# Optimization experiments

Hardware: AMD Instinct MI355X
Metric: run time of the kernel (lower is better)

The kernel has to match this reference:

```python
import jax, jax.numpy as jnp
import numpy as np

SIGMA = 16
P = 2 * SIGMA + 1  # 33x33 patch
OUT = 128          # feature_extractor.output_size
DN = ('NCHW', 'OIHW', 'NCHW')


def setup_inputs() -> dict:
    key = jax.random.key(0)
    ks = jax.random.split(key, 10)
    B, K, H, W = 4, 64, 256, 256
    images_ground = jax.random.normal(ks[0], (B, 3, H, W), jnp.float32)
    images_satellite = jax.random.normal(ks[1], (B, 3, H, W), jnp.float32)
    # normalized keypoints kept in interior so sigma-window crops stay in-bounds
    keypoints_ground = 0.2 + 0.6 * jax.random.uniform(ks[2], (B, K, 2), jnp.float32)
    keypoints_satellite = 0.2 + 0.6 * jax.random.uniform(ks[3], (B, K, 2), jnp.float32)
    # small CNN feature extractor params (conv 3->32 s1, conv 32->64 s2, GAP, linear 64->OUT)
    w1 = jax.random.normal(ks[4], (32, 3, 3, 3), jnp.float32) * 0.1
    b1 = jnp.zeros((32,), jnp.float32)
    w2 = jax.random.normal(ks[5], (64, 32, 3, 3), jnp.float32) * 0.05
    b2 = jnp.zeros((64,), jnp.float32)
    wl = jax.random.normal(ks[6], (OUT, 64), jnp.float32) * 0.1
    bl = jnp.zeros((OUT,), jnp.float32)
    return dict(images_ground=images_ground, images_satellite=images_satellite,
                keypoints_ground=keypoints_ground, keypoints_satellite=keypoints_satellite,
                w1=w1, b1=b1, w2=w2, b2=b2, wl=wl, bl=bl, num_samples=K)


def _cnn(x, w1, b1, w2, b2, wl, bl):
    # x: [M, 3, P, P] -> [M, OUT]
    h = jax.lax.conv_general_dilated(x, w1, (1, 1), 'VALID', dimension_numbers=DN)
    h = jax.nn.relu(h + b1[None, :, None, None])
    h = jax.lax.conv_general_dilated(h, w2, (2, 2), 'VALID', dimension_numbers=DN)
    h = jax.nn.relu(h + b2[None, :, None, None])
    h = h.mean(axis=(2, 3))  # global average pool -> [M, 64]
    return h @ wl.T + bl


def _crop_all(images, kps_px):
    # images: [B,3,H,W]; kps_px: [N,2] pixel (x, y) coords -> patches [N,B,3,P,P]
    B = images.shape[0]
    hw = images.shape[-1]
    starts = jnp.clip(jnp.floor(kps_px).astype(jnp.int32) - SIGMA, 0, hw - P)
    def one(st):
        return jax.lax.dynamic_slice(images, (0, 0, st[1], st[0]), (B, 3, P, P))
    return jax.vmap(one)(starts)


def reference(images_ground, images_satellite, keypoints_ground, keypoints_satellite,
              w1, b1, w2, b2, wl, bl, num_samples):
    kg = (keypoints_ground * images_ground.shape[-1]).reshape(-1, 2)   # [N,2]
    ksat = (keypoints_satellite * images_satellite.shape[-1]).reshape(-1, 2)
    pg = _crop_all(images_ground, kg)        # [N,B,3,P,P]
    ps = _crop_all(images_satellite, ksat)   # [N,B,3,P,P]
    N, B = pg.shape[0], pg.shape[1]
    fg = _cnn(pg.reshape(N * B, 3, P, P), w1, b1, w2, b2, wl, bl)
    fs = _cnn(ps.reshape(N * B, 3, P, P), w1, b1, w2, b2, wl, bl)
    fg = fg.reshape(N, B, OUT).transpose(1, 0, 2)  # features_ground [B,N,OUT]
    fs = fs.reshape(N, B, OUT).transpose(1, 0, 2)
    return jnp.mean((fg - fs) ** 2)
```

## Files before the change

kernel.cpp:

```cpp
#include <hip/hip_runtime.h>

#define HW   256
#define Pp   33
#define PPAD 36
#define OUTF 128
#define SIG  16

#define KCP   40
#define PLROW (2 * 16 * KCP)
#define PLSZ  (6 * PLROW)
#define IMS   40

#define WS_W1FH 0
#define WS_W1FL 512
#define WS_BHI  1024
#define WS_BLO  10240
#define WS_WLT  19456

typedef __attribute__((ext_vector_type(8))) short v8s;
typedef __attribute__((ext_vector_type(4))) short v4s;
typedef __attribute__((ext_vector_type(4))) float f32x4;

__device__ __forceinline__ unsigned short f2bf_rne(float x) {
  unsigned u = __float_as_uint(x);
  unsigned r = (u + 0x7FFFu + ((u >> 16) & 1u)) >> 16;
  return (unsigned short)r;
}
__device__ __forceinline__ float bf2f(unsigned short h) {
  return __uint_as_float(((unsigned)h) << 16);
}

__global__ __launch_bounds__(256) void prep_kernel(
    const float* __restrict__ w1, const float* __restrict__ w2,
    const float* __restrict__ wl, float* __restrict__ ws,
    float* __restrict__ out) {
  int t = blockIdx.x * 256 + threadIdx.x;
  int stride = gridDim.x * 256;
  if (blockIdx.x == 0 && threadIdx.x == 0) out[0] = 0.0f;
  unsigned short* w1h = (unsigned short*)(ws + WS_W1FH);
  unsigned short* w1lo = (unsigned short*)(ws + WS_W1FL);
  for (int i = t; i < 1024; i += stride) {
    int j  = i & 7;
    int l  = (i >> 3) & 63;
    int nt = i >> 9;
    int k  = 8 * (l >> 4) + j;
    int ch = 16 * nt + (l & 15);
    float v = (k < 27) ? w1[ch * 27 + k] : 0.0f;
    unsigned short h = f2bf_rne(v);
    w1h[i]  = h;
    w1lo[i] = f2bf_rne(v - bf2f(h));
  }
  unsigned short* bhi = (unsigned short*)(ws + WS_BHI);
  unsigned short* blo = (unsigned short*)(ws + WS_BLO);
  for (int i = t; i < 18432; i += stride) {
    int j  = i & 7;
    int l  = (i >> 3) & 63;
    int w  = (i >> 9) & 3;
    int tp = i >> 11;
    int ch = w * 16 + (l & 15);
    int kc = ((l >> 4) << 3) + j;
    int ky = tp / 3, kx = tp - ky * 3;
    float v = w2[ch * 288 + kc * 9 + ky * 3 + kx];
    unsigned short h = f2bf_rne(v);
    bhi[i] = h;
    blo[i] = f2bf_rne(v - bf2f(h));
  }
  for (int i = t; i < 8192; i += stride) {
    int o = i & 127, ii = i >> 7;
    ws[WS_WLT + i] = wl[o * 64 + ii];
  }
}

__global__ __launch_bounds__(256) void patch_cnn_kernel(
    const float* __restrict__ imgG, const float* __restrict__ imgS,
    const float* __restrict__ kpG,  const float* __restrict__ kpS,
    const float* __restrict__ b1g,  const float* __restrict__ b2g,
    const float* __restrict__ blg,  const float* __restrict__ ws,
    float* __restrict__ out) {
  __shared__ __align__(16) unsigned short patch[3 * Pp * PPAD];
  __shared__ __align__(16) unsigned short imcol[4][32 * IMS];
  __shared__ __align__(16) unsigned short hiP[PLSZ];
  __shared__ float gapv[64];
  __shared__ float fstash[OUTF];
  __shared__ float lred[4];

  const int bid  = blockIdx.x;
  const int n    = bid >> 2;
  const int b    = bid & 3;
  const int tid  = threadIdx.x;
  const int wave = tid >> 6;
  const int lane = tid & 63;

  const int m16 = lane & 15;
  const int qq  = lane >> 4;
  const int mt  = wave & 1;
  const int nt  = wave >> 1;

  const int bm = tid & 31;
  const int kq = tid >> 5;
  int  boff[4];
  bool bval[4];
#pragma unroll
  for (int j = 0; j < 4; ++j) {
    int k = 4 * kq + j;
    bval[j] = (k < 27);
    int kk = bval[j] ? k : 0;
    int ci = kk / 9, r2 = kk - ci * 9, ky = r2 / 3, kx = r2 - ky * 3;
    boff[j] = (ci * Pp + ky) * PPAD + bm + kx;
  }

  const v8s w1hF = ((const v8s*)((const unsigned short*)(ws + WS_W1FH)))[nt * 64 + lane];
  const v8s w1lF = ((const v8s*)((const unsigned short*)(ws + WS_W1FL)))[nt * 64 + lane];
  const float4 b1q = *(const float4*)&b1g[16 * nt + 4 * qq];

  const v8s* bhW = (const v8s*)((const unsigned short*)(ws + WS_BHI)) + (wave * 64 + lane);
  const v8s* blW = (const v8s*)((const unsigned short*)(ws + WS_BLO)) + (wave * 64 + lane);
  const float b2v = b2g[wave * 16 + m16];

  auto build_row = [&](int r, int d) {
    unsigned short h[4];
#pragma unroll
    for (int j = 0; j < 4; ++j)
      h[j] = bval[j] ? patch[boff[j] + r * PPAD] : (unsigned short)0;
    unsigned w0 = (unsigned)h[0] | ((unsigned)h[1] << 16);
    unsigned w1_ = (unsigned)h[2] | ((unsigned)h[3] << 16);
    *(uint2*)&imcol[d][bm * IMS + 4 * kq] = make_uint2(w0, w1_);
  };

  auto conv1_pair = [&](int bp, int r0) {
#pragma unroll
    for (int rr = 0; rr < 2; ++rr) {
      const int row = r0 + rr;
      if (row <= 30) {
        int sl = row % 6;
        v8s af = *(const v8s*)&imcol[2 * bp + rr][(16 * mt + m16) * IMS + 8 * qq];
        f32x4 a1 = {0.f, 0.f, 0.f, 0.f};
        a1 = __builtin_amdgcn_mfma_f32_16x16x32_bf16(w1hF, af, a1, 0, 0, 0);
        a1 = __builtin_amdgcn_mfma_f32_16x16x32_bf16(w1lF, af, a1, 0, 0, 0);
        const int x = 16 * mt + m16;
        v4s hv;
        hv[0] = (short)f2bf_rne(fmaxf(a1.x + b1q.x, 0.f));
        hv[1] = (short)f2bf_rne(fmaxf(a1.y + b1q.y, 0.f));
        hv[2] = (short)f2bf_rne(fmaxf(a1.z + b1q.z, 0.f));
        hv[3] = (short)f2bf_rne(fmaxf(a1.w + b1q.w, 0.f));
        const int idx = ((sl * 2 + (x & 1)) * 16 + (x >> 1)) * KCP + 16 * nt + 4 * qq;
        *(v4s*)&hiP[idx] = hv;
      }
    }
  };

  float dd = 0.0f;

#pragma unroll 1
  for (int side = 0; side < 2; ++side) {
    const float* img = side ? imgS : imgG;
    const float* kp  = side ? kpS : kpG;

    int sx = (int)floorf(kp[n * 2 + 0] * 256.0f) - SIG;
    int sy = (int)floorf(kp[n * 2 + 1] * 256.0f) - SIG;
    sx = min(max(sx, 0), HW - Pp);
    sy = min(max(sy, 0), HW - Pp);

    for (int i = tid; i < (3 * Pp * PPAD) / 2; i += 256) {
      int e  = 2 * i;
      int ci = e / (Pp * PPAD);
      int r2 = e - ci * (Pp * PPAD);
      int r  = r2 / PPAD;
      int cc = r2 - r * PPAD;
      float vx = 0.f, vy = 0.f;
      const float* rowp = &img[((b * 3 + ci) * HW + (sy + r)) * HW + sx];
      if (cc < 32) { float2 v = *(const float2*)(rowp + cc); vx = v.x; vy = v.y; }
      else if (cc == 32) { vx = rowp[32]; }
      unsigned pk = (unsigned)f2bf_rne(vx) | ((unsigned)f2bf_rne(vy) << 16);
      *(unsigned*)&patch[e] = pk;
    }
    __syncthreads();

    build_row(0, 0); build_row(1, 1);
    __syncthreads();
    conv1_pair(0, 0); build_row(2, 2); build_row(3, 3);
    __syncthreads();
    conv1_pair(1, 2); build_row(4, 0); build_row(5, 1);
    __syncthreads();

    float gapAcc = 0.0f;
    int s0 = 0;
    int bp = 0;
#pragma unroll 1
    for (int y2 = 0; y2 < 15; ++y2) {
      const int r0 = 2 * y2 + 4;
      if (r0 <= 30) conv1_pair(bp, r0);
      const int r1 = 2 * y2 + 6;
      if (r1 <= 30) {
        build_row(r1, 2 * (bp ^ 1));
        build_row(min(r1 + 1, 30), 2 * (bp ^ 1) + 1);
      }
      f32x4 acc = {0.f, 0.f, 0.f, 0.f};
#pragma unroll
      for (int ky = 0; ky < 3; ++ky) {
        int sk = s0 + ky; if (sk >= 6) sk -= 6;
#pragma unroll
        for (int kx = 0; kx < 3; ++kx) {
          const int p = kx & 1;
          int cp = m16 + (kx >> 1); if (cp > 15) cp = 15;
          const int idx = ((sk * 2 + p) * 16 + cp) * KCP + qq * 8;
          v8s ah = *(const v8s*)&hiP[idx];
          const int tp = ky * 3 + kx;
          v8s bh = bhW[tp * 256];
          v8s bl = blW[tp * 256];
          acc = __builtin_amdgcn_mfma_f32_16x16x32_bf16(ah, bh, acc, 0, 0, 0);
          acc = __builtin_amdgcn_mfma_f32_16x16x32_bf16(ah, bl, acc, 0, 0, 0);
        }
      }
      {
        float s = fmaxf(acc.x + b2v, 0.f) + fmaxf(acc.y + b2v, 0.f) +
                  fmaxf(acc.z + b2v, 0.f);
        if (qq < 3) s += fmaxf(acc.w + b2v, 0.f);
        gapAcc += s;
      }
      __syncthreads();
      s0 += 2; if (s0 >= 6) s0 -= 6;
      bp ^= 1;
    }

    gapAcc += __shfl_down(gapAcc, 32, 64);
    gapAcc += __shfl_down(gapAcc, 16, 64);
    if (lane < 16) gapv[wave * 16 + m16] = gapAcc * (1.0f / 225.0f);
    __syncthreads();

    if (tid < OUTF) {
      float f = blg[tid];
#pragma unroll 8
      for (int i = 0; i < 64; ++i) f = fmaf(gapv[i], ws[WS_WLT + i * OUTF + tid], f);
      if (side == 0) fstash[tid] = f;
      else { float d = f - fstash[tid]; dd = d * d; }
    }
    __syncthreads();
  }

  dd += __shfl_down(dd, 32, 64);
  dd += __shfl_down(dd, 16, 64);
  dd += __shfl_down(dd, 8, 64);
  dd += __shfl_down(dd, 4, 64);
  dd += __shfl_down(dd, 2, 64);
  dd += __shfl_down(dd, 1, 64);
  if (lane == 0) lred[wave] = dd;
  __syncthreads();
  if (tid == 0) {
    float s = (lred[0] + lred[1]) + (lred[2] + lred[3]);
    atomicAdd(out, s * (1.0f / 131072.0f));
  }
}

extern "C" void kernel_launch(void* const* d_in, const int* in_sizes, int n_in,
                              void* d_out, int out_size, void* d_ws, size_t ws_size,
                              hipStream_t stream) {
  const float* imgG = (const float*)d_in[0];
  const float* imgS = (const float*)d_in[1];
  const float* kpG  = (const float*)d_in[2];
  const float* kpS  = (const float*)d_in[3];
  const float* w1   = (const float*)d_in[4];
  const float* b1   = (const float*)d_in[5];
  const float* w2   = (const float*)d_in[6];
  const float* b2   = (const float*)d_in[7];
  const float* wl   = (const float*)d_in[8];
  const float* bl   = (const float*)d_in[9];
  float* ws  = (float*)d_ws;
  float* out = (float*)d_out;

  hipLaunchKernelGGL(prep_kernel, dim3(32), dim3(256), 0, stream, w1, w2, wl, ws, out);
  hipLaunchKernelGGL(patch_cnn_kernel, dim3(1024), dim3(256), 0, stream,
                     imgG, imgS, kpG, kpS, b1, b2, bl, ws, out);
}
```

Before: 152.5 us.

## Assign conv2 output rows round-robin to waves, each computing all channels

Conv2 work was split across waves by output-channel tile, so every wave computed its 16 channels on every output row. Now each wave handles every fourth output row and computes all 64 output channels, with four accumulators sharing one A-fragment load. Per-wave partial GAP sums are combined through a new shared buffer and an extra barrier. This trades fewer A reads from LDS per wave for load imbalance: the 15 rows split unevenly across four waves, one wave does the full MFMA chain each iteration while the others sit idle at the barrier, and register pressure goes up.

```diff
diff --git a/kernel.cpp b/kernel.cpp
--- a/kernel.cpp
+++ b/kernel.cpp
@@ -80,6 +80,7 @@
   __shared__ __align__(16) unsigned short patch[3 * Pp * PPAD];
   __shared__ __align__(16) unsigned short imcol[4][32 * IMS];
   __shared__ __align__(16) unsigned short hiP[PLSZ];
+  __shared__ float gapP[4 * 64];
   __shared__ float gapv[64];
   __shared__ float fstash[OUTF];
   __shared__ float lred[4];
@@ -113,9 +114,11 @@
   const v8s w1lF = ((const v8s*)((const unsigned short*)(ws + WS_W1FL)))[nt * 64 + lane];
   const float4 b1q = *(const float4*)&b1g[16 * nt + 4 * qq];
 
-  const v8s* bhW = (const v8s*)((const unsigned short*)(ws + WS_BHI)) + (wave * 64 + lane);
-  const v8s* blW = (const v8s*)((const unsigned short*)(ws + WS_BLO)) + (wave * 64 + lane);
-  const float b2v = b2g[wave * 16 + m16];
+  const v8s* bhB = (const v8s*)((const unsigned short*)(ws + WS_BHI)) + lane;
+  const v8s* blB = (const v8s*)((const unsigned short*)(ws + WS_BLO)) + lane;
+  float b2q[4];
+#pragma unroll
+  for (int bt = 0; bt < 4; ++bt) b2q[bt] = b2g[16 * bt + m16];
 
   auto build_row = [&](int r, int d) {
     unsigned short h[4];
@@ -183,7 +186,7 @@
     conv1_pair(1, 2); build_row(4, 0); build_row(5, 1);
     __syncthreads();
 
-    float gapAcc = 0.0f;
+    float gAcc[4] = {0.f, 0.f, 0.f, 0.f};
     int s0 = 0;
     int bp = 0;
 #pragma unroll 1
@@ -195,37 +198,57 @@
         build_row(r1, 2 * (bp ^ 1));
         build_row(min(r1 + 1, 30), 2 * (bp ^ 1) + 1);
       }
-      f32x4 acc = {0.f, 0.f, 0.f, 0.f};
-#pragma unroll
-      for (int ky = 0; ky < 3; ++ky) {
-        int sk = s0 + ky; if (sk >= 6) sk -= 6;
-#pragma unroll
-        for (int kx = 0; kx < 3; ++kx) {
-          const int p = kx & 1;
-          int cp = m16 + (kx >> 1); if (cp > 15) cp = 15;
-          const int idx = ((sk * 2 + p) * 16 + cp) * KCP + qq * 8;
-          v8s ah = *(const v8s*)&hiP[idx];
-          const int tp = ky * 3 + kx;
-          v8s bh = bhW[tp * 256];
-          v8s bl = blW[tp * 256];
-          acc = __builtin_amdgcn_mfma_f32_16x16x32_bf16(ah, bh, acc, 0, 0, 0);
-          acc = __builtin_amdgcn_mfma_f32_16x16x32_bf16(ah, bl, acc, 0, 0, 0);
+      if ((y2 & 3) == wave) {
+        f32x4 acc0 = {0.f,0.f,0.f,0.f}, acc1 = {0.f,0.f,0.f,0.f};
+        f32x4 acc2 = {0.f,0.f,0.f,0.f}, acc3 = {0.f,0.f,0.f,0.f};
+#pragma unroll
+        for (int ky = 0; ky < 3; ++ky) {
+          int sk = s0 + ky; if (sk >= 6) sk -= 6;
+#pragma unroll
+          for (int kx = 0; kx < 3; ++kx) {
+            const int p = kx & 1;
+            int cp = m16 + (kx >> 1); if (cp > 15) cp = 15;
+            const int idx = ((sk * 2 + p) * 16 + cp) * KCP + qq * 8;
+            v8s ah = *(const v8s*)&hiP[idx];
+            const int tp = ky * 3 + kx;
+            const int fb = tp * 4 * 64;
+            acc0 = __builtin_amdgcn_mfma_f32_16x16x32_bf16(ah, bhB[fb], acc0, 0, 0, 0);
+            acc0 = __builtin_amdgcn_mfma_f32_16x16x32_bf16(ah, blB[fb], acc0, 0, 0, 0);
+            acc1 = __builtin_amdgcn_mfma_f32_16x16x32_bf16(ah, bhB[fb + 64], acc1, 0, 0, 0);
+            acc1 = __builtin_amdgcn_mfma_f32_16x16x32_bf16(ah, blB[fb + 64], acc1, 0, 0, 0);
+            acc2 = __builtin_amdgcn_mfma_f32_16x16x32_bf16(ah, bhB[fb + 128], acc2, 0, 0, 0);
+            acc2 = __builtin_amdgcn_mfma_f32_16x16x32_bf16(ah, blB[fb + 128], acc2, 0, 0, 0);
+            acc3 = __builtin_amdgcn_mfma_f32_16x16x32_bf16(ah, bhB[fb + 192], acc3, 0, 0, 0);
+            acc3 = __builtin_amdgcn_mfma_f32_16x16x32_bf16(ah, blB[fb + 192], acc3, 0, 0, 0);
+          }
         }
-      }
-      {
-        float s = fmaxf(acc.x + b2v, 0.f) + fmaxf(acc.y + b2v, 0.f) +
-                  fmaxf(acc.z + b2v, 0.f);
-        if (qq < 3) s += fmaxf(acc.w + b2v, 0.f);
-        gapAcc += s;
+        f32x4 av[4] = {acc0, acc1, acc2, acc3};
+#pragma unroll
+        for (int bt = 0; bt < 4; ++bt) {
+          float s = fmaxf(av[bt].x + b2q[bt], 0.f) + fmaxf(av[bt].y + b2q[bt], 0.f) +
+                    fmaxf(av[bt].z + b2q[bt], 0.f);
+          if (qq < 3) s += fmaxf(av[bt].w + b2q[bt], 0.f);
+          gAcc[bt] += s;
+        }
       }
       __syncthreads();
       s0 += 2; if (s0 >= 6) s0 -= 6;
       bp ^= 1;
     }
 
-    gapAcc += __shfl_down(gapAcc, 32, 64);
-    gapAcc += __shfl_down(gapAcc, 16, 64);
-    if (lane < 16) gapv[wave * 16 + m16] = gapAcc * (1.0f / 225.0f);
+#pragma unroll
+    for (int bt = 0; bt < 4; ++bt) {
+      gAcc[bt] += __shfl_down(gAcc[bt], 32, 64);
+      gAcc[bt] += __shfl_down(gAcc[bt], 16, 64);
+    }
+    if (lane < 16) {
+#pragma unroll
+      for (int bt = 0; bt < 4; ++bt) gapP[wave * 64 + bt * 16 + lane] = gAcc[bt];
+    }
+    __syncthreads();
+    if (tid < 64)
+      gapv[tid] = (gapP[tid] + gapP[64 + tid] + gapP[128 + tid] + gapP[192 + tid]) *
+                  (1.0f / 225.0f);
     __syncthreads();
 
     if (tid < OUTF) {
```

Result: slower. 537.1 us (+252.3%).
